# Kernel optimization log

Measured on AMD Instinct MI355X. Metric: run time of the kernel, lower is better.

Reference implementation:

```python
import jax, jax.numpy as jnp
import numpy as np

H = 8       # heads
DH = 64     # dim_head
EPS = 1e-5  # LayerNorm eps (torch default)


def _ln(x, g, b):
    m = x.mean(-1, keepdims=True)
    v = x.var(-1, keepdims=True)
    return (x - m) / jnp.sqrt(v + EPS) * g + b


def setup_inputs() -> dict:
    key = jax.random.key(0)
    ks = jax.random.split(key, 8)
    B, N, D = 2, 2048, 512
    s = lambda k, shape: jax.random.normal(k, shape, jnp.float32) * 0.02
    return {
        "q": jax.random.normal(ks[0], (B, N, D), jnp.float32),
        "k": jax.random.normal(ks[1], (B, N, D), jnp.float32),
        "v": jax.random.normal(ks[2], (B, N, D), jnp.float32),
        "ln_g": jnp.ones((D,), jnp.float32),
        "ln_b": jnp.zeros((D,), jnp.float32),
        "W_in": s(ks[3], (H * DH, D)),          # Linear(dim, inner_dim, bias=False)
        "wp_w1": s(ks[4], (DH, 2 * DH)),         # Linear(2*dim_head, dim_head)
        "wp_b1": jnp.zeros((DH,), jnp.float32),
        "wp_ln_g": jnp.ones((DH,), jnp.float32),
        "wp_ln_b": jnp.zeros((DH,), jnp.float32),
        "wp_w2": s(ks[5], (1, DH)),              # Linear(dim_head, 1)
        "wp_b2": jnp.zeros((1,), jnp.float32),
        "W_out": s(ks[6], (D, H * DH)),          # Linear(inner_dim, dim)
        "b_out": jnp.zeros((D,), jnp.float32),
    }


def reference(q, k, v, ln_g, ln_b, W_in, wp_w1, wp_b1, wp_ln_g, wp_ln_b,
              wp_w2, wp_b2, W_out, b_out):
    B, N, D = q.shape

    def proj(t):
        x = _ln(t, ln_g, ln_b) @ W_in.T                 # [B, N, H*DH]
        return x.reshape(B, N, H, DH).transpose(2, 0, 1, 3)  # [H, B, N, DH]

    fq, fk, fv = proj(q), proj(k), proj(v)

    # cosine similarity component
    dots = jnp.einsum('hbnd,hbmd->hbnm', fq, fk)        # [H, B, N, N]
    qn = jnp.linalg.norm(fq, axis=-1)                   # [H, B, N]
    kn = jnp.linalg.norm(fk, axis=-1)
    cosine = dots / (qn[..., :, None] * kn[..., None, :])

    # mean-centered covariance component
    qc = fq - fq.mean(-1, keepdims=True)
    kc = fk - fk.mean(-1, keepdims=True)
    cov = jnp.einsum('hbnd,hbmd->hbnm', qc, kc) / DH    # [H, B, N, N]

    # dynamic per-head blend weight
    qg = fq.mean((1, 2))                                # [H, DH]
    kg = fk.mean((1, 2))
    feat = jnp.concatenate([qg, kg], axis=-1)           # [H, 2*DH]
    hid = jax.nn.relu(_ln(feat @ wp_w1.T + wp_b1, wp_ln_g, wp_ln_b))
    w = jax.nn.sigmoid(hid @ wp_w2.T + wp_b2)           # [H, 1]
    w = w.reshape(H, 1, 1, 1)

    blend = (1.0 - w) * cosine + w * cov                # no softmax in cosine variant
    out = jnp.einsum('hbnm,hbmd->hbnd', blend, fv)      # [H, B, N, DH]
    out = out.transpose(1, 2, 0, 3).reshape(B, N, H * DH)
    return out @ W_out.T + b_out
```

## Files before the change

kernel.cpp:

```cpp
#include <hip/hip_runtime.h>
#include <stdint.h>

#define CH 8
#define CDH 64
#define CB 2
#define CN 2048
#define CD 512

typedef float f32x4 __attribute__((ext_vector_type(4)));
typedef __bf16 bf16x8 __attribute__((ext_vector_type(8)));
typedef unsigned short u16;

#define MFMA(a, b, c) __builtin_amdgcn_mfma_f32_16x16x32_bf16((a), (b), (c), 0, 0, 0)
#define GLOAD16(g, l)                                                              \
  __builtin_amdgcn_global_load_lds((const __attribute__((address_space(1))) void*)(g), \
                                   (__attribute__((address_space(3))) void*)(l), 16, 0, 0)

__device__ __forceinline__ u16 f2bf(float f) {
  union { float f; unsigned u; } c; c.f = f;
  return (u16)((c.u + 0x7FFFu + ((c.u >> 16) & 1u)) >> 16);
}
__device__ __forceinline__ float bf2f(u16 h) {
  union { unsigned u; float f; } c; c.u = ((unsigned)h) << 16;
  return c.f;
}

__global__ __launch_bounds__(256) void ln_convw_kernel(const float* __restrict__ q,
                                                       const float* __restrict__ k,
                                                       const float* __restrict__ v,
                                                       const float* __restrict__ g,
                                                       const float* __restrict__ bb,
                                                       u16* __restrict__ xln,
                                                       const float* __restrict__ wi_f,
                                                       const float* __restrict__ wo_f,
                                                       u16* __restrict__ wi,
                                                       u16* __restrict__ wo) {
  int row = blockIdx.x;
  int tid = threadIdx.x;
  if (row >= 12288) {
    int i = (row - 12288) * 256 + tid;
    wi[i] = f2bf(wi_f[i]);
    wo[i] = f2bf(wo_f[i]);
    return;
  }
  int t = row >> 12;
  int rr = row & 4095;
  const float* src = (t == 0 ? q : (t == 1 ? k : v)) + (size_t)rr * CD;
  float x0 = src[tid], x1 = src[tid + 256];
  float s = x0 + x1, s2 = x0 * x0 + x1 * x1;
#pragma unroll
  for (int m = 1; m < 64; m <<= 1) { s += __shfl_xor(s, m); s2 += __shfl_xor(s2, m); }
  __shared__ float red[8];
  int w = tid >> 6;
  if ((tid & 63) == 0) { red[w] = s; red[4 + w] = s2; }
  __syncthreads();
  s = red[0] + red[1] + red[2] + red[3];
  s2 = red[4] + red[5] + red[6] + red[7];
  float mean = s * (1.f / 512.f);
  float var = s2 * (1.f / 512.f) - mean * mean;
  float rstd = rsqrtf(var + 1e-5f);
  u16* dst = xln + (size_t)row * CD;
  dst[tid]       = f2bf((x0 - mean) * rstd * g[tid] + bb[tid]);
  dst[tid + 256] = f2bf((x1 - mean) * rstd * g[tid + 256] + bb[tid + 256]);
}

__global__ __launch_bounds__(256) void gemm1(const u16* __restrict__ A,
                                             const u16* __restrict__ Bt,
                                             u16* __restrict__ F0,
                                             float* __restrict__ iqn,
                                             float* __restrict__ ikn,
                                             float* __restrict__ qgp,
                                             float* __restrict__ kgp,
                                             u16* __restrict__ fkT,
                                             u16* __restrict__ fvT) {
  __shared__ u16 S[4][8192];
#define AL_(s) (S[s])
#define BL_(s) (S[2 + (s)])
  int tm = blockIdx.x * 128, tn = blockIdx.y * 128;
  int tid = threadIdx.x;
  int w = tid >> 6, l = tid & 63;
  int wr = w >> 1, wc = w & 1;
  int lo = l & 15, hi = l >> 4;

  f32x4 zz = {0.f, 0.f, 0.f, 0.f};
  f32x4 acc[4][4];
#pragma unroll
  for (int mi = 0; mi < 4; mi++)
#pragma unroll
    for (int ni = 0; ni < 4; ni++) acc[mi][ni] = zz;

  int rowA = 8 * w + (l >> 3);
  int sl = l & 7;

#pragma unroll
  for (int i = 0; i < 4; i++) {
    int rl = rowA + 32 * i;
    int sp = sl ^ (rl & 7);
    GLOAD16(A + (size_t)(tm + rl) * CD + sp * 8, (char*)AL_(0) + w * 1024 + i * 4096);
    GLOAD16(Bt + (size_t)(tn + rl) * CD + sp * 8, (char*)BL_(0) + w * 1024 + i * 4096);
  }
  __syncthreads();

  int cur = 0;
  for (int kt = 0; kt < 8; ++kt) {
    if (kt + 1 < 8) {
      int nxt = cur ^ 1;
#pragma unroll
      for (int i = 0; i < 4; i++) {
        int rl = rowA + 32 * i;
        int sp = sl ^ (rl & 7);
        GLOAD16(A + (size_t)(tm + rl) * CD + (kt + 1) * 64 + sp * 8,
                (char*)AL_(nxt) + w * 1024 + i * 4096);
        GLOAD16(Bt + (size_t)(tn + rl) * CD + (kt + 1) * 64 + sp * 8,
                (char*)BL_(nxt) + w * 1024 + i * 4096);
      }
    }
    const u16* Ac = AL_(cur);
    const u16* Bc = BL_(cur);
#pragma unroll
    for (int kk = 0; kk < 2; kk++) {
      bf16x8 af[4], bfr[4];
#pragma unroll
      for (int mi = 0; mi < 4; mi++) {
        int row = wr * 64 + mi * 16 + lo;
        int slot = (hi + 4 * kk) ^ (row & 7);
        af[mi] = *(const bf16x8*)&Ac[row * 64 + slot * 8];
      }
#pragma unroll
      for (int ni = 0; ni < 4; ni++) {
        int row = wc * 64 + ni * 16 + lo;
        int slot = (hi + 4 * kk) ^ (row & 7);
        bfr[ni] = *(const bf16x8*)&Bc[row * 64 + slot * 8];
      }
#pragma unroll
      for (int mi = 0; mi < 4; mi++)
#pragma unroll
        for (int ni = 0; ni < 4; ni++)
          acc[mi][ni] = MFMA(af[mi], bfr[ni], acc[mi][ni]);
    }
    if (kt + 1 < 8) {
      __syncthreads();
      cur ^= 1;
    }
  }

  int tblk = blockIdx.x;
  int h = blockIdx.y * 2 + wc;
  if (tblk < 32) {
#pragma unroll
    for (int mi = 0; mi < 4; mi++)
#pragma unroll
      for (int rg = 0; rg < 4; rg++) {
        float s2 = 0.f;
#pragma unroll
        for (int ni = 0; ni < 4; ni++) {
          float vv = acc[mi][ni][rg];
          s2 += vv * vv;
        }
#pragma unroll
        for (int m = 1; m < 16; m <<= 1) s2 += __shfl_xor(s2, m);
        if (lo == 0) {
          int rloc = tm + wr * 64 + mi * 16 + hi * 4 + rg;
          int b = rloc >> 11, n = rloc & 2047;
          iqn[((size_t)h * 2 + b) * CN + n] = rsqrtf(s2);
        }
      }
    float cs[4];
#pragma unroll
    for (int ni = 0; ni < 4; ni++) {
      float s = 0.f;
#pragma unroll
      for (int mi = 0; mi < 4; mi++)
#pragma unroll
        for (int rg = 0; rg < 4; rg++) s += acc[mi][ni][rg];
      s += __shfl_xor(s, 16);
      s += __shfl_xor(s, 32);
      cs[ni] = s;
    }
    __syncthreads();
    float* redl = (float*)&S[0][0];
    if (hi == 0)
#pragma unroll
      for (int ni = 0; ni < 4; ni++) redl[((wr * 2 + wc) * 4 + ni) * 16 + lo] = cs[ni];
    __syncthreads();
    if (wr == 0 && hi == 0) {
#pragma unroll
      for (int ni = 0; ni < 4; ni++) {
        float vsum = redl[((0 * 2 + wc) * 4 + ni) * 16 + lo] +
                     redl[((1 * 2 + wc) * 4 + ni) * 16 + lo];
        qgp[(tblk * 8 + h) * 64 + ni * 16 + lo] = vsum;
      }
    }
#pragma unroll
    for (int mi = 0; mi < 4; mi++)
#pragma unroll
      for (int ni = 0; ni < 4; ni++) {
        int gcol = tn + wc * 64 + ni * 16 + lo;
#pragma unroll
        for (int rg = 0; rg < 4; rg++) {
          int rowg = tm + wr * 64 + mi * 16 + hi * 4 + rg;
          F0[(size_t)rowg * CD + gcol] = f2bf(acc[mi][ni][rg]);
        }
      }
  } else {
    bool isk = tblk < 64;
    u16* dstT = isk ? fkT : fvT;
    int rloc0 = tm - (isk ? 4096 : 8192);
    int bb2 = rloc0 >> 11, n0 = rloc0 & 2047;
    float csk[4];
    if (isk) {
#pragma unroll
      for (int mi = 0; mi < 4; mi++)
#pragma unroll
        for (int rg = 0; rg < 4; rg++) {
          float s2 = 0.f;
#pragma unroll
          for (int ni = 0; ni < 4; ni++) {
            float vv = acc[mi][ni][rg];
            s2 += vv * vv;
          }
#pragma unroll
          for (int m = 1; m < 16; m <<= 1) s2 += __shfl_xor(s2, m);
          if (lo == 0) {
            int n = n0 + wr * 64 + mi * 16 + hi * 4 + rg;
            ikn[((size_t)h * 2 + bb2) * CN + n] = rsqrtf(s2);
          }
        }
#pragma unroll
      for (int ni = 0; ni < 4; ni++) {
        float s = 0.f;
#pragma unroll
        for (int mi = 0; mi < 4; mi++)
#pragma unroll
          for (int rg = 0; rg < 4; rg++) s += acc[mi][ni][rg];
        s += __shfl_xor(s, 16);
        s += __shfl_xor(s, 32);
        csk[ni] = s;
      }
    }
    __syncthreads();
    u16* Sf = &S[0][0];
    int reg = wc * 2 + wr;
#pragma unroll
    for (int mi = 0; mi < 4; mi++)
#pragma unroll
      for (int ni = 0; ni < 4; ni++) {
        int d = ni * 16 + lo;
        int m0 = mi * 16 + hi * 4;
        u16 t4[4];
#pragma unroll
        for (int rg = 0; rg < 4; rg++) t4[rg] = f2bf(acc[mi][ni][rg]);
        int off = (reg * 64 + d) * 64 + (m0 ^ ((d & 7) << 3));
        *(uint2*)&Sf[off] = *(const uint2*)t4;
      }
    __syncthreads();
    {
      int head = tid >> 7, c = tid & 127;
      int hg = blockIdx.y * 2 + head;
      size_t base = ((size_t)(hg * 2 + bb2)) * 64 * CN;
#pragma unroll
      for (int p = 0; p < 8; p++) {
        int flat = p * 128 + c;
        int d = flat >> 4, mc = flat & 15;
        int wr2 = mc >> 3, m64 = (mc & 7) * 8;
        int off = ((head * 2 + wr2) * 64 + d) * 64 + (m64 ^ ((d & 7) << 3));
        bf16x8 vv = *(const bf16x8*)&Sf[off];
        *(bf16x8*)&dstT[base + (size_t)d * CN + n0 + mc * 8] = vv;
      }
    }
    if (isk) {
      __syncthreads();
      float* redl = (float*)&S[0][0];
      if (hi == 0)
#pragma unroll
        for (int ni = 0; ni < 4; ni++) redl[((wr * 2 + wc) * 4 + ni) * 16 + lo] = csk[ni];
      __syncthreads();
      if (wr == 0 && hi == 0) {
#pragma unroll
        for (int ni = 0; ni < 4; ni++) {
          float vsum = redl[((0 * 2 + wc) * 4 + ni) * 16 + lo] +
                       redl[((1 * 2 + wc) * 4 + ni) * 16 + lo];
          kgp[((tblk - 32) * 8 + h) * 64 + ni * 16 + lo] = vsum;
        }
      }
    }
  }
#undef AL_
#undef BL_
}

__global__ __launch_bounds__(256) void gemm_M(const u16* __restrict__ fkT,
                                              const u16* __restrict__ fvT,
                                              const float* __restrict__ ikn,
                                              float* __restrict__ Mpart) {
  int bid = blockIdx.x;
  int hb = bid & 15, ms = bid >> 4;
  int tid = threadIdx.x, w = tid >> 6, l = tid & 63;
  int lo = l & 15, hi = l >> 4;

  __shared__ u16 GM[6][4096];
#define AK_(s) (GM[s])
#define AKH_(s) (GM[2 + (s)])
#define BV_(s) (GM[4 + (s)])

  const u16* Ab = fkT + (size_t)hb * 64 * CN;
  const u16* Vb = fvT + (size_t)hb * 64 * CN;
  const float* ikb = ikn + (size_t)hb * CN;

  f32x4 zz = {0.f, 0.f, 0.f, 0.f};
  f32x4 acc[2][4];
#pragma unroll
  for (int mat = 0; mat < 2; mat++)
#pragma unroll
    for (int dt = 0; dt < 4; dt++) acc[mat][dt] = zz;

  int rls = 8 * w + (l >> 3);
  int sls = l & 7;

  bf16x8 areg[2];
  f32x4 ikreg[2][2];

  auto STAGEGL = [&](int kt, int slot) {
    int mc = ms * 512 + kt * 64;
#pragma unroll
    for (int i = 0; i < 2; i++) {
      int row = rls + 32 * i;
      int sp = sls ^ (row & 7);
      GLOAD16(Ab + (size_t)row * CN + mc + sp * 8, (char*)AK_(slot) + w * 1024 + i * 4096);
      GLOAD16(Vb + (size_t)row * CN + mc + sp * 8, (char*)BV_(slot) + w * 1024 + i * 4096);
    }
  };
  auto LOADA = [&](int kt) {
    int mc = ms * 512 + kt * 64;
#pragma unroll
    for (int i = 0; i < 2; i++) {
      int row = rls + 32 * i;
      int sp = sls ^ (row & 7);
      areg[i] = *(const bf16x8*)&Ab[(size_t)row * CN + mc + sp * 8];
      ikreg[i][0] = *(const f32x4*)&ikb[mc + sp * 8];
      ikreg[i][1] = *(const f32x4*)&ikb[mc + sp * 8 + 4];
    }
  };
  auto WRITEA = [&](int slot) {
#pragma unroll
    for (int i = 0; i < 2; i++) {
      u16 outp[8];
#pragma unroll
      for (int j = 0; j < 4; j++) outp[j] = f2bf((float)areg[i][j] * ikreg[i][0][j]);
#pragma unroll
      for (int j = 0; j < 4; j++) outp[4 + j] = f2bf((float)areg[i][4 + j] * ikreg[i][1][j]);
      *(bf16x8*)((char*)AKH_(slot) + w * 1024 + i * 4096 + l * 16) = *(const bf16x8*)outp;
    }
  };

  LOADA(0);
  STAGEGL(0, 0);
  WRITEA(0);
  __syncthreads();

  int cur = 0;
  for (int kt = 0; kt < 8; ++kt) {
    if (kt + 1 < 8) {
      LOADA(kt + 1);
      STAGEGL(kt + 1, cur ^ 1);
    }
#pragma unroll
    for (int kk = 0; kk < 2; kk++) {
      int arow = w * 16 + lo;
      int aslot = (hi + 4 * kk) ^ (arow & 7);
      bf16x8 af = *(const bf16x8*)&AK_(cur)[arow * 64 + aslot * 8];
      bf16x8 afh = *(const bf16x8*)&AKH_(cur)[arow * 64 + aslot * 8];
#pragma unroll
      for (int dt = 0; dt < 4; dt++) {
        int brow = dt * 16 + lo;
        int bslot = (hi + 4 * kk) ^ (brow & 7);
        bf16x8 bv = *(const bf16x8*)&BV_(cur)[brow * 64 + bslot * 8];
        acc[0][dt] = MFMA(afh, bv, acc[0][dt]);
        acc[1][dt] = MFMA(af, bv, acc[1][dt]);
      }
    }
    if (kt + 1 < 8) {
      WRITEA(cur ^ 1);
      __syncthreads();
      cur ^= 1;
    }
  }

  float* outp = Mpart + ((size_t)(hb * 4 + ms)) * 8192;
#pragma unroll
  for (int mat = 0; mat < 2; mat++)
#pragma unroll
    for (int dt = 0; dt < 4; dt++) {
      int d = dt * 16 + lo;
#pragma unroll
      for (int rg = 0; rg < 4; rg++) {
        int j = mat * 64 + w * 16 + hi * 4 + rg;
        outp[j * 64 + d] = acc[mat][dt][rg];
      }
    }
#undef AK_
#undef AKH_
#undef BV_
}

__global__ __launch_bounds__(256) void reduceM_mlp(const float* __restrict__ Mpart,
                                                   const float* __restrict__ qgp,
                                                   const float* __restrict__ kgp,
                                                   const float* __restrict__ w1,
                                                   const float* __restrict__ b1,
                                                   const float* __restrict__ lng,
                                                   const float* __restrict__ lnb,
                                                   const float* __restrict__ w2,
                                                   const float* __restrict__ b2,
                                                   u16* __restrict__ Bmat) {
  int hb = blockIdx.x;
  int h = hb >> 1;
  int tid = threadIdx.x;
  __shared__ float qg[64], kg[64], abg[3];
  if (tid < 64) {
    float s1 = 0.f, s2 = 0.f;
#pragma unroll
    for (int c = 0; c < 32; c++) {
      s1 += qgp[(c * 8 + h) * 64 + tid];
      s2 += kgp[(c * 8 + h) * 64 + tid];
    }
    qg[tid] = s1 * (1.f / 4096.f);
    kg[tid] = s2 * (1.f / 4096.f);
    float acc = b1[tid];
#pragma unroll 8
    for (int i = 0; i < 64; i++)
      acc += qg[i] * w1[tid * 128 + i] + kg[i] * w1[tid * 128 + 64 + i];
    float t1 = acc, t2 = acc * acc;
#pragma unroll
    for (int m = 1; m < 64; m <<= 1) { t1 += __shfl_xor(t1, m); t2 += __shfl_xor(t2, m); }
    float mean = t1 * (1.f / 64.f);
    float var = t2 * (1.f / 64.f) - mean * mean;
    float y = (acc - mean) * rsqrtf(var + 1e-5f) * lng[tid] + lnb[tid];
    float hid = fmaxf(y, 0.f);
    float t = hid * w2[tid];
#pragma unroll
    for (int m = 1; m < 64; m <<= 1) t += __shfl_xor(t, m);
    float wv = 1.f / (1.f + expf(-(t + b2[0])));
    if (tid == 0) { abg[0] = 1.f - wv; abg[1] = wv * (1.f / 64.f); abg[2] = wv; }
  }
  __syncthreads();
  float alpha = abg[0], beta = abg[1], gamma = abg[2];

  __shared__ float Ms[128 * 65];
  __shared__ float S2s[64];
#pragma unroll
  for (int e = 0; e < 32; e++) {
    int idx = e * 256 + tid;
    int j = idx >> 6, d = idx & 63;
    float s = 0.f;
#pragma unroll
    for (int ms = 0; ms < 4; ms++)
      s += Mpart[((size_t)(hb * 4 + ms)) * 8192 + idx];
    Ms[j * 65 + d] = s;
  }
  __syncthreads();
  if (tid < 64) {
    float s = 0.f;
#pragma unroll
    for (int i = 0; i < 64; i++) s += Ms[(64 + i) * 65 + tid];
    S2s[tid] = s;
  }
  __syncthreads();
#pragma unroll
  for (int e = 0; e < 32; e++) {
    int idx = e * 256 + tid;
    int jr = idx >> 6, ic = idx & 63;
    float v;
    if (jr < 64) v = alpha * Ms[ic * 65 + jr];
    else {
      int d = jr - 64;
      v = beta * Ms[(64 + ic) * 65 + d] - (gamma * (1.f / 4096.f)) * S2s[d];
    }
    Bmat[(size_t)hb * 8192 + idx] = f2bf(v);
  }
}

__global__ __launch_bounds__(256) void gemm_out(const u16* __restrict__ F0,
                                                const u16* __restrict__ Bmat,
                                                const float* __restrict__ iqn,
                                                u16* __restrict__ A2) {
  int bid = blockIdx.x;
  int hb = bid >> 4, qt = bid & 15;
  int b = hb & 1, h = hb >> 1;
  int tid = threadIdx.x, w = tid >> 6, l = tid & 63;
  int lo = l & 15, hi = l >> 4;
  int qbase = qt * 128;

  const u16* Bm = Bmat + (size_t)hb * 8192;
  bf16x8 bm[8][2];
#pragma unroll
  for (int jt = 0; jt < 8; jt++)
#pragma unroll
    for (int kk = 0; kk < 2; kk++)
      bm[jt][kk] = *(const bf16x8*)&Bm[(jt * 16 + lo) * 64 + hi * 8 + kk * 32];

  f32x4 zz = {0.f, 0.f, 0.f, 0.f};
  f32x4 acc[2][8];
#pragma unroll
  for (int f = 0; f < 2; f++)
#pragma unroll
    for (int jt = 0; jt < 8; jt++) acc[f][jt] = zz;

#pragma unroll
  for (int f = 0; f < 2; f++) {
    const u16* qp = F0 + ((size_t)(b * CN + qbase + w * 32 + f * 16 + lo)) * CD +
                    h * 64 + hi * 8;
    bf16x8 a0 = *(const bf16x8*)qp;
    bf16x8 a1 = *(const bf16x8*)(qp + 32);
#pragma unroll
    for (int jt = 0; jt < 8; jt++) {
      acc[f][jt] = MFMA(a0, bm[jt][0], acc[f][jt]);
      acc[f][jt] = MFMA(a1, bm[jt][1], acc[f][jt]);
    }
  }

  const float* iqn_hb = iqn + (size_t)hb * CN;
#pragma unroll
  for (int f = 0; f < 2; f++) {
    float iqv[4];
    int nb = qbase + w * 32 + f * 16 + hi * 4;
#pragma unroll
    for (int rg = 0; rg < 4; rg++) iqv[rg] = iqn_hb[nb + rg];
#pragma unroll
    for (int jt = 0; jt < 4; jt++) {
      int d = jt * 16 + lo;
#pragma unroll
      for (int rg = 0; rg < 4; rg++) {
        float vout = iqv[rg] * acc[f][jt][rg] + acc[f][jt + 4][rg];
        int n = nb + rg;
        A2[((size_t)(b * CN + n)) * CD + h * 64 + d] = f2bf(vout);
      }
    }
  }
}

__global__ __launch_bounds__(256) void gemm2(const u16* __restrict__ A,
                                             const u16* __restrict__ Bt,
                                             const float* __restrict__ bias,
                                             float* __restrict__ Cout) {
  __shared__ u16 Al[2][128 * 64];
  __shared__ u16 Bl[2][128 * 64];
  int tm = blockIdx.x * 128, tn = blockIdx.y * 128;
  int tid = threadIdx.x;
  int w = tid >> 6, l = tid & 63;
  int wr = w >> 1, wc = w & 1;
  int lo = l & 15, hi = l >> 4;

  f32x4 zz = {0.f, 0.f, 0.f, 0.f};
  f32x4 acc[4][4];
#pragma unroll
  for (int mi = 0; mi < 4; mi++)
#pragma unroll
    for (int ni = 0; ni < 4; ni++) acc[mi][ni] = zz;

  int rowA = 8 * w + (l >> 3);
  int sl = l & 7;

#pragma unroll
  for (int i = 0; i < 4; i++) {
    int rl = rowA + 32 * i;
    int sp = sl ^ (rl & 7);
    GLOAD16(A + (size_t)(tm + rl) * CD + sp * 8, (char*)Al[0] + w * 1024 + i * 4096);
    GLOAD16(Bt + (size_t)(tn + rl) * CD + sp * 8, (char*)Bl[0] + w * 1024 + i * 4096);
  }
  __syncthreads();

  int cur = 0;
  for (int kt = 0; kt < 8; ++kt) {
    if (kt + 1 < 8) {
      int nxt = cur ^ 1;
#pragma unroll
      for (int i = 0; i < 4; i++) {
        int rl = rowA + 32 * i;
        int sp = sl ^ (rl & 7);
        GLOAD16(A + (size_t)(tm + rl) * CD + (kt + 1) * 64 + sp * 8,
                (char*)Al[nxt] + w * 1024 + i * 4096);
        GLOAD16(Bt + (size_t)(tn + rl) * CD + (kt + 1) * 64 + sp * 8,
                (char*)Bl[nxt] + w * 1024 + i * 4096);
      }
    }
    const u16* Ac = Al[cur];
    const u16* Bc = Bl[cur];
#pragma unroll
    for (int kk = 0; kk < 2; kk++) {
      bf16x8 af[4], bfr[4];
#pragma unroll
      for (int mi = 0; mi < 4; mi++) {
        int row = wr * 64 + mi * 16 + lo;
        int slot = (hi + 4 * kk) ^ (row & 7);
        af[mi] = *(const bf16x8*)&Ac[row * 64 + slot * 8];
      }
#pragma unroll
      for (int ni = 0; ni < 4; ni++) {
        int row = wc * 64 + ni * 16 + lo;
        int slot = (hi + 4 * kk) ^ (row & 7);
        bfr[ni] = *(const bf16x8*)&Bc[row * 64 + slot * 8];
      }
#pragma unroll
      for (int mi = 0; mi < 4; mi++)
#pragma unroll
        for (int ni = 0; ni < 4; ni++)
          acc[mi][ni] = MFMA(af[mi], bfr[ni], acc[mi][ni]);
    }
    if (kt + 1 < 8) {
      __syncthreads();
      cur ^= 1;
    }
  }
#pragma unroll
  for (int mi = 0; mi < 4; mi++)
#pragma unroll
    for (int ni = 0; ni < 4; ni++) {
      int col = tn + wc * 64 + ni * 16 + lo;
      float bv = bias[col];
#pragma unroll
      for (int rg = 0; rg < 4; rg++) {
        int rowg = tm + wr * 64 + mi * 16 + hi * 4 + rg;
        Cout[(size_t)rowg * CD + col] = acc[mi][ni][rg] + bv;
      }
    }
}

extern "C" void kernel_launch(void* const* d_in, const int* in_sizes, int n_in,
                              void* d_out, int out_size, void* d_ws, size_t ws_size,
                              hipStream_t stream) {
  const float* q = (const float*)d_in[0];
  const float* k = (const float*)d_in[1];
  const float* v = (const float*)d_in[2];
  const float* ln_g = (const float*)d_in[3];
  const float* ln_b = (const float*)d_in[4];
  const float* W_in = (const float*)d_in[5];
  const float* wp_w1 = (const float*)d_in[6];
  const float* wp_b1 = (const float*)d_in[7];
  const float* wp_lng = (const float*)d_in[8];
  const float* wp_lnb = (const float*)d_in[9];
  const float* wp_w2 = (const float*)d_in[10];
  const float* wp_b2 = (const float*)d_in[11];
  const float* W_out = (const float*)d_in[12];
  const float* b_out = (const float*)d_in[13];

  char* ws = (char*)d_ws;
  u16* xln = (u16*)(ws + 0);
  u16* F0 = (u16*)(ws + 12582912);
  u16* Wi = (u16*)(ws + 16777216);
  u16* Wo = (u16*)(ws + 17301504);
  u16* fkT = (u16*)(ws + 17825792);
  u16* fvT = (u16*)(ws + 22020096);
  u16* A2 = (u16*)(ws + 26214400);
  float* iqn = (float*)(ws + 30408704);
  float* ikn = (float*)(ws + 30539776);
  float* qgp = (float*)(ws + 30670848);
  float* kgp = (float*)(ws + 30736384);
  float* Mpart = (float*)(ws + 30801920);
  u16* Bmat = (u16*)(ws + 32899072);

  ln_convw_kernel<<<13312, 256, 0, stream>>>(q, k, v, ln_g, ln_b, xln,
                                             W_in, W_out, Wi, Wo);
  gemm1<<<dim3(96, 4), 256, 0, stream>>>(xln, Wi, F0, iqn, ikn, qgp, kgp, fkT, fvT);
  gemm_M<<<64, 256, 0, stream>>>(fkT, fvT, ikn, Mpart);
  reduceM_mlp<<<16, 256, 0, stream>>>(Mpart, qgp, kgp, wp_w1, wp_b1,
                                      wp_lng, wp_lnb, wp_w2, wp_b2, Bmat);
  gemm_out<<<256, 256, 0, stream>>>(F0, Bmat, iqn, A2);
  gemm2<<<dim3(32, 4), 256, 0, stream>>>(A2, Wo, b_out, (float*)d_out);
}
```

Measured before the change: 62.69 us.

## Fuse per-head attention output GEMM into final output projection

Merges gemm_out and gemm2 into one kernel. Each 128x128 output tile computes the per-head A tile (F0 times Bmat, scaled by the inverse q norm) straight into LDS, then multiplies it with a double-buffered Wo slice, looping over heads as the K dimension. This drops the A2 global round trip and one launch. In exchange, each of the 4 column blocks recomputes the per-head A tile (4x redundant MFMA work on that stage), and the grid shrinks to 128 blocks with extra barriers per head.

```diff
diff --git a/kernel.cpp b/kernel.cpp
--- a/kernel.cpp
+++ b/kernel.cpp
@@ -480,72 +480,16 @@
   }
 }
 
-__global__ __launch_bounds__(256) void gemm_out(const u16* __restrict__ F0,
-                                                const u16* __restrict__ Bmat,
-                                                const float* __restrict__ iqn,
-                                                u16* __restrict__ A2) {
-  int bid = blockIdx.x;
-  int hb = bid >> 4, qt = bid & 15;
-  int b = hb & 1, h = hb >> 1;
-  int tid = threadIdx.x, w = tid >> 6, l = tid & 63;
-  int lo = l & 15, hi = l >> 4;
-  int qbase = qt * 128;
-
-  const u16* Bm = Bmat + (size_t)hb * 8192;
-  bf16x8 bm[8][2];
-#pragma unroll
-  for (int jt = 0; jt < 8; jt++)
-#pragma unroll
-    for (int kk = 0; kk < 2; kk++)
-      bm[jt][kk] = *(const bf16x8*)&Bm[(jt * 16 + lo) * 64 + hi * 8 + kk * 32];
-
-  f32x4 zz = {0.f, 0.f, 0.f, 0.f};
-  f32x4 acc[2][8];
-#pragma unroll
-  for (int f = 0; f < 2; f++)
-#pragma unroll
-    for (int jt = 0; jt < 8; jt++) acc[f][jt] = zz;
-
-#pragma unroll
-  for (int f = 0; f < 2; f++) {
-    const u16* qp = F0 + ((size_t)(b * CN + qbase + w * 32 + f * 16 + lo)) * CD +
-                    h * 64 + hi * 8;
-    bf16x8 a0 = *(const bf16x8*)qp;
-    bf16x8 a1 = *(const bf16x8*)(qp + 32);
-#pragma unroll
-    for (int jt = 0; jt < 8; jt++) {
-      acc[f][jt] = MFMA(a0, bm[jt][0], acc[f][jt]);
-      acc[f][jt] = MFMA(a1, bm[jt][1], acc[f][jt]);
-    }
-  }
-
-  const float* iqn_hb = iqn + (size_t)hb * CN;
-#pragma unroll
-  for (int f = 0; f < 2; f++) {
-    float iqv[4];
-    int nb = qbase + w * 32 + f * 16 + hi * 4;
-#pragma unroll
-    for (int rg = 0; rg < 4; rg++) iqv[rg] = iqn_hb[nb + rg];
-#pragma unroll
-    for (int jt = 0; jt < 4; jt++) {
-      int d = jt * 16 + lo;
-#pragma unroll
-      for (int rg = 0; rg < 4; rg++) {
-        float vout = iqv[rg] * acc[f][jt][rg] + acc[f][jt + 4][rg];
-        int n = nb + rg;
-        A2[((size_t)(b * CN + n)) * CD + h * 64 + d] = f2bf(vout);
-      }
-    }
-  }
-}
-
-__global__ __launch_bounds__(256) void gemm2(const u16* __restrict__ A,
-                                             const u16* __restrict__ Bt,
-                                             const float* __restrict__ bias,
-                                             float* __restrict__ Cout) {
-  __shared__ u16 Al[2][128 * 64];
-  __shared__ u16 Bl[2][128 * 64];
+__global__ __launch_bounds__(256) void gemm_out2(const u16* __restrict__ F0,
+                                                 const u16* __restrict__ Bmat,
+                                                 const float* __restrict__ iqn,
+                                                 const u16* __restrict__ Wo,
+                                                 const float* __restrict__ bias,
+                                                 float* __restrict__ Cout) {
+  __shared__ u16 Atile[8192];
+  __shared__ u16 Bl[2][8192];
   int tm = blockIdx.x * 128, tn = blockIdx.y * 128;
+  int b = tm >> 11, n0 = tm & 2047;
   int tid = threadIdx.x;
   int w = tid >> 6, l = tid & 63;
   int wr = w >> 1, wc = w & 1;
@@ -561,31 +505,72 @@
   int rowA = 8 * w + (l >> 3);
   int sl = l & 7;
 
-#pragma unroll
-  for (int i = 0; i < 4; i++) {
-    int rl = rowA + 32 * i;
-    int sp = sl ^ (rl & 7);
-    GLOAD16(A + (size_t)(tm + rl) * CD + sp * 8, (char*)Al[0] + w * 1024 + i * 4096);
-    GLOAD16(Bt + (size_t)(tn + rl) * CD + sp * 8, (char*)Bl[0] + w * 1024 + i * 4096);
-  }
-  __syncthreads();
-
-  int cur = 0;
-  for (int kt = 0; kt < 8; ++kt) {
-    if (kt + 1 < 8) {
-      int nxt = cur ^ 1;
-#pragma unroll
-      for (int i = 0; i < 4; i++) {
-        int rl = rowA + 32 * i;
-        int sp = sl ^ (rl & 7);
-        GLOAD16(A + (size_t)(tm + rl) * CD + (kt + 1) * 64 + sp * 8,
-                (char*)Al[nxt] + w * 1024 + i * 4096);
-        GLOAD16(Bt + (size_t)(tn + rl) * CD + (kt + 1) * 64 + sp * 8,
-                (char*)Bl[nxt] + w * 1024 + i * 4096);
-      }
-    }
-    const u16* Ac = Al[cur];
-    const u16* Bc = Bl[cur];
+  auto STAGE_WO = [&](int h, int slot) {
+#pragma unroll
+    for (int i = 0; i < 4; i++) {
+      int rl = rowA + 32 * i;
+      int sp = sl ^ (rl & 7);
+      GLOAD16(Wo + (size_t)(tn + rl) * CD + h * 64 + sp * 8,
+              (char*)Bl[slot] + w * 1024 + i * 4096);
+    }
+  };
+
+  f32x4 accA[2][8];
+  auto COMPUTEA = [&](int h) {
+    int hb = h * 2 + b;
+    const u16* Bm = Bmat + (size_t)hb * 8192;
+    bf16x8 bm[8][2];
+#pragma unroll
+    for (int jt = 0; jt < 8; jt++)
+#pragma unroll
+      for (int kk = 0; kk < 2; kk++)
+        bm[jt][kk] = *(const bf16x8*)&Bm[(jt * 16 + lo) * 64 + hi * 8 + kk * 32];
+#pragma unroll
+    for (int f = 0; f < 2; f++)
+#pragma unroll
+      for (int jt = 0; jt < 8; jt++) accA[f][jt] = zz;
+#pragma unroll
+    for (int f = 0; f < 2; f++) {
+      const u16* qp = F0 + ((size_t)(tm + w * 32 + f * 16 + lo)) * CD + h * 64 + hi * 8;
+      bf16x8 a0 = *(const bf16x8*)qp;
+      bf16x8 a1 = *(const bf16x8*)(qp + 32);
+#pragma unroll
+      for (int jt = 0; jt < 8; jt++) {
+        accA[f][jt] = MFMA(a0, bm[jt][0], accA[f][jt]);
+        accA[f][jt] = MFMA(a1, bm[jt][1], accA[f][jt]);
+      }
+    }
+  };
+  auto WRITE_ATILE = [&](int h) {
+    int hb = h * 2 + b;
+    const float* iqn_hb = iqn + (size_t)hb * CN;
+#pragma unroll
+    for (int f = 0; f < 2; f++) {
+      float iqv[4];
+      int rb = w * 32 + f * 16 + hi * 4;
+#pragma unroll
+      for (int rg = 0; rg < 4; rg++) iqv[rg] = iqn_hb[n0 + rb + rg];
+#pragma unroll
+      for (int jt = 0; jt < 4; jt++) {
+        int d = jt * 16 + lo;
+#pragma unroll
+        for (int rg = 0; rg < 4; rg++) {
+          float vout = iqv[rg] * accA[f][jt][rg] + accA[f][jt + 4][rg];
+          int row = rb + rg;
+          Atile[row * 64 + (((d >> 3) ^ (row & 7)) << 3) + (d & 7)] = f2bf(vout);
+        }
+      }
+    }
+  };
+
+  STAGE_WO(0, 0);
+  COMPUTEA(0);
+
+  for (int h = 0; h < 8; ++h) {
+    __syncthreads();
+    if (h + 1 < 8) STAGE_WO(h + 1, (h + 1) & 1);
+    WRITE_ATILE(h);
+    __syncthreads();
 #pragma unroll
     for (int kk = 0; kk < 2; kk++) {
       bf16x8 af[4], bfr[4];
@@ -593,13 +578,13 @@
       for (int mi = 0; mi < 4; mi++) {
         int row = wr * 64 + mi * 16 + lo;
         int slot = (hi + 4 * kk) ^ (row & 7);
-        af[mi] = *(const bf16x8*)&Ac[row * 64 + slot * 8];
+        af[mi] = *(const bf16x8*)&Atile[row * 64 + slot * 8];
       }
 #pragma unroll
       for (int ni = 0; ni < 4; ni++) {
         int row = wc * 64 + ni * 16 + lo;
         int slot = (hi + 4 * kk) ^ (row & 7);
-        bfr[ni] = *(const bf16x8*)&Bc[row * 64 + slot * 8];
+        bfr[ni] = *(const bf16x8*)&Bl[h & 1][row * 64 + slot * 8];
       }
 #pragma unroll
       for (int mi = 0; mi < 4; mi++)
@@ -607,11 +592,9 @@
         for (int ni = 0; ni < 4; ni++)
           acc[mi][ni] = MFMA(af[mi], bfr[ni], acc[mi][ni]);
     }
-    if (kt + 1 < 8) {
-      __syncthreads();
-      cur ^= 1;
-    }
-  }
+    if (h + 1 < 8) COMPUTEA(h + 1);
+  }
+
 #pragma unroll
   for (int mi = 0; mi < 4; mi++)
 #pragma unroll
@@ -651,13 +634,12 @@
   u16* Wo = (u16*)(ws + 17301504);
   u16* fkT = (u16*)(ws + 17825792);
   u16* fvT = (u16*)(ws + 22020096);
-  u16* A2 = (u16*)(ws + 26214400);
-  float* iqn = (float*)(ws + 30408704);
-  float* ikn = (float*)(ws + 30539776);
-  float* qgp = (float*)(ws + 30670848);
-  float* kgp = (float*)(ws + 30736384);
-  float* Mpart = (float*)(ws + 30801920);
-  u16* Bmat = (u16*)(ws + 32899072);
+  float* iqn = (float*)(ws + 26214400);
+  float* ikn = (float*)(ws + 26345472);
+  float* qgp = (float*)(ws + 26476544);
+  float* kgp = (float*)(ws + 26542080);
+  float* Mpart = (float*)(ws + 26607616);
+  u16* Bmat = (u16*)(ws + 28704768);
 
   ln_convw_kernel<<<13312, 256, 0, stream>>>(q, k, v, ln_g, ln_b, xln,
                                              W_in, W_out, Wi, Wo);
@@ -665,6 +647,5 @@
   gemm_M<<<64, 256, 0, stream>>>(fkT, fvT, ikn, Mpart);
   reduceM_mlp<<<16, 256, 0, stream>>>(Mpart, qgp, kgp, wp_w1, wp_b1,
                                       wp_lng, wp_lnb, wp_w2, wp_b2, Bmat);
-  gemm_out<<<256, 256, 0, stream>>>(F0, Bmat, iqn, A2);
-  gemm2<<<dim3(32, 4), 256, 0, stream>>>(A2, Wo, b_out, (float*)d_out);
-}
+  gemm_out2<<<dim3(32, 4), 256, 0, stream>>>(F0, Bmat, iqn, Wo, b_out, (float*)d_out);
+}
```

Measured after the change: 80.88 us. 29.0% more time.
